# Performance work log

Hardware: AMD Instinct MI355X
Metric: run time of the kernel (lower is better)

## Reference

```python
import jax, jax.numpy as jnp
import numpy as np

N, K, E = 50000, 8, 800000
HID, OUT, DIM_PE, DIM_IN, DIM_EMB = 64, 16, 16, 64, 128

def setup_inputs() -> dict:
    key = jax.random.key(0)
    ks = jax.random.split(key, 16)
    s = 0.05
    inp = {
        "eigvecs": jax.random.normal(ks[0], (N, K), jnp.float32),
        "x": jax.random.normal(ks[1], (N, DIM_IN), jnp.float32),
        "edge_index": jax.random.randint(ks[2], (2, E), 0, N, jnp.int32),
        "batch_index": jnp.sort(jax.random.randint(ks[3], (N,), 0, 8, jnp.int32)),
        # GIN layer 0: MLP(1 -> HID, 1 layer) == single Linear
        "W0": jax.random.normal(ks[4], (1, HID), jnp.float32) * s,
        "b0": jnp.zeros((HID,), jnp.float32),
        # GIN layer 1: MLP(HID -> HID, 1 layer)
        "W1": jax.random.normal(ks[5], (HID, HID), jnp.float32) * s,
        "b1": jnp.zeros((HID,), jnp.float32),
        # GIN layer 2: MLP(HID -> HID -> OUT, 2 layers, relu between)
        "W2a": jax.random.normal(ks[6], (HID, HID), jnp.float32) * s,
        "b2a": jnp.zeros((HID,), jnp.float32),
        "W2b": jax.random.normal(ks[7], (HID, OUT), jnp.float32) * s,
        "b2b": jnp.zeros((OUT,), jnp.float32),
        # rho: MLP(OUT*K -> HID -> DIM_PE, 2 layers)
        "Wr1": jax.random.normal(ks[8], (OUT * K, HID), jnp.float32) * s,
        "br1": jnp.zeros((HID,), jnp.float32),
        "Wr2": jax.random.normal(ks[9], (HID, DIM_PE), jnp.float32) * s,
        "br2": jnp.zeros((DIM_PE,), jnp.float32),
        # linear_x: dim_in -> dim_emb - dim_pe
        "Wx": jax.random.normal(ks[10], (DIM_IN, DIM_EMB - DIM_PE), jnp.float32) * s,
        "bx": jnp.zeros((DIM_EMB - DIM_PE,), jnp.float32),
    }
    return inp

def reference(eigvecs, x, edge_index, batch_index,
              W0, b0, W1, b1, W2a, b2a, W2b, b2b,
              Wr1, br1, Wr2, br2, Wx, bx):
    src, dst = edge_index[0], edge_index[1]

    def agg(h):
        # GINConv sum aggregation: out[i] = h[i] + sum_{(j->i) in E} h[j]  (eps=0)
        return h + jax.ops.segment_sum(h[src], dst, num_segments=N)

    def enc(p):
        # p: [N, K, C]; Linear acts on last dim, message passing on node dim 0
        h = agg(p) @ W0 + b0                       # GINConv(MLP 1-layer): [N,K,HID]
        h = agg(h) @ W1 + b1                       # GINConv(MLP 1-layer)
        m = agg(h)
        return jax.nn.relu(m @ W2a + b2a) @ W2b + b2b  # GINConv(MLP 2-layer): [N,K,OUT]

    # pos_enc = eigvecs.unsqueeze(-1), NaN -> 0
    pos = jnp.nan_to_num(eigvecs)[:, :, None]      # [N,K,1]
    pe = enc(pos) + enc(-pos)                      # sign-invariant sum: [N,K,OUT]
    pe = pe.reshape(N, K * OUT)                    # [N, K*OUT]
    pe = jax.nn.relu(pe @ Wr1 + br1) @ Wr2 + br2   # rho MLP: [N, DIM_PE]

    h = x.astype(jnp.float32) @ Wx + bx            # expand_x linear: [N, DIM_EMB-DIM_PE]
    return jnp.concatenate([h, pe], axis=1)        # [N, DIM_EMB]
```

## Files before the change

### kernel.cpp

```cpp
#include <hip/hip_runtime.h>

__global__ void smallvec_k(const float* __restrict__ W0, const float* __restrict__ b0,
                           const float* __restrict__ W1, const float* __restrict__ b1,
                           const float* __restrict__ W2a, float* __restrict__ SV) {
  __shared__ float w01[64], g[64];
  int j = threadIdx.x;
  float a = 0.f, bg = 0.f;
  for (int i = 0; i < 64; ++i) { float w = W1[i*64 + j]; a += W0[i]*w; bg += b0[i]*w; }
  w01[j] = a; g[j] = bg;
  __syncthreads();
  float w012 = 0.f, P = 0.f, Q = 0.f;
  for (int i = 0; i < 64; ++i) { float w = W2a[i*64 + j]; w012 += w01[i]*w; P += g[i]*w; Q += b1[i]*w; }
  SV[j] = w012; SV[64 + j] = P; SV[128 + j] = Q;
}

__global__ void zero_k(int* __restrict__ p, int n) {
  int i = blockIdx.x * blockDim.x + threadIdx.x;
  if (i < n) p[i] = 0;
}

__global__ void hist_k(const int* __restrict__ ei, int* __restrict__ cnt, int E) {
  int e = blockIdx.x * blockDim.x + threadIdx.x;
  if (e < E) atomicAdd(&cnt[ei[E + e]], 1);
}

__global__ void scan_k(int* __restrict__ ptr, int* __restrict__ cur, int N) {
  __shared__ int sums[256];
  int t = threadIdx.x;
  int chunk = (N + 255) / 256;
  int lo = t * chunk, hi = lo + chunk; if (hi > N) hi = N; if (lo > N) lo = N;
  int s = 0;
  for (int i = lo; i < hi; ++i) s += ptr[i];
  sums[t] = s;
  __syncthreads();
  for (int off = 1; off < 256; off <<= 1) {
    int v = (t >= off) ? sums[t - off] : 0;
    __syncthreads();
    sums[t] += v;
    __syncthreads();
  }
  int run = sums[t] - s;
  for (int i = lo; i < hi; ++i) {
    int c = ptr[i];
    ptr[i] = run; cur[i] = run;
    run += c;
  }
  if (t == 255) ptr[N] = run;
}

__global__ void fill_k(const int* __restrict__ ei, int* __restrict__ cur,
                       int* __restrict__ csr, int E) {
  int e = blockIdx.x * blockDim.x + threadIdx.x;
  if (e >= E) return;
  int s = ei[e], d = ei[E + e];
  int pos = atomicAdd(&cur[d], 1);
  csr[pos] = s;
}

#define RED16(v) { v += __shfl_down(v, 8, 16); v += __shfl_down(v, 4, 16); \
                   v += __shfl_down(v, 2, 16); v += __shfl_down(v, 1, 16); }
#define NANFIX4(u) { u.x = (u.x!=u.x)?0.f:u.x; u.y = (u.y!=u.y)?0.f:u.y; \
                     u.z = (u.z!=u.z)?0.f:u.z; u.w = (u.w!=u.w)?0.f:u.w; }

template<int MODE>
__global__ __launch_bounds__(256) void aggv_k(
    const int* __restrict__ ptr, const int* __restrict__ csr,
    const float* __restrict__ Fin, const float* __restrict__ Din,
    float* __restrict__ Fout, float* __restrict__ Dout, int N) {
  int g = blockIdx.x * 16 + (threadIdx.x >> 4);
  int t = threadIdx.x & 15;
  if (g >= N) return;
  int lo = ptr[g], hi = ptr[g + 1];
  float a0=0.f,a1=0.f,a2=0.f,a3=0.f,a4=0.f,a5=0.f,a6=0.f,a7=0.f,dd=0.f;
  for (int j = lo + t; j < hi; j += 16) {
    int s = csr[j];
    const float* r = Fin + (size_t)s * 8;
    float4 u0 = *(const float4*)r;
    float4 u1 = *(const float4*)(r + 4);
    if (MODE == 0) { NANFIX4(u0); NANFIX4(u1); }
    a0 += u0.x; a1 += u0.y; a2 += u0.z; a3 += u0.w;
    a4 += u1.x; a5 += u1.y; a6 += u1.z; a7 += u1.w;
    if (MODE == 1) dd += Din[s];
  }
  RED16(a0); RED16(a1); RED16(a2); RED16(a3);
  RED16(a4); RED16(a5); RED16(a6); RED16(a7);
  if (MODE == 1) RED16(dd);
  if (t == 0) {
    const float* r = Fin + (size_t)g * 8;
    float4 s0 = *(const float4*)r;
    float4 s1 = *(const float4*)(r + 4);
    if (MODE == 0) { NANFIX4(s0); NANFIX4(s1); }
    float4 o0 = { a0 + s0.x, a1 + s0.y, a2 + s0.z, a3 + s0.w };
    float4 o1 = { a4 + s1.x, a5 + s1.y, a6 + s1.z, a7 + s1.w };
    *(float4*)(Fout + (size_t)g * 8)     = o0;
    *(float4*)(Fout + (size_t)g * 8 + 4) = o1;
    if (MODE == 0) Dout[g] = 1.f + (float)(hi - lo);
    if (MODE == 1) Dout[g] = Din[g] + dd;
  }
}

__global__ __launch_bounds__(256) void pe_k(
    const float* __restrict__ B3, const float* __restrict__ D1, const float* __restrict__ D2,
    const float* __restrict__ SV, const float* __restrict__ b2a,
    const float* __restrict__ W2b, const float* __restrict__ b2b,
    const float* __restrict__ Wr1, const float* __restrict__ br1,
    const float* __restrict__ Wr2, const float* __restrict__ br2,
    float* __restrict__ out, int N) {
  __shared__ float vbuf[4][8][68];
  __shared__ float pebuf[4][128];
  __shared__ float zbuf[4][64];
  int wid  = threadIdx.x >> 6;
  int lane = threadIdx.x & 63;
  int n = blockIdx.x * 4 + wid;
  bool active = (n < N);
  float d1 = 0.f, d2 = 0.f;
  if (active) { d1 = D1[n]; d2 = D2[n]; }
  float w012 = SV[lane], P = SV[64 + lane], Q = SV[128 + lane];
  float Ej = d2 * P + d1 * Q + b2a[lane];
  if (active) {
    #pragma unroll
    for (int k = 0; k < 8; ++k) {
      float s = B3[(size_t)n*8 + k];
      float t = s * w012;
      vbuf[wid][k][lane] = fmaxf(t + Ej, 0.f) + fmaxf(Ej - t, 0.f);
    }
  }
  __syncthreads();
  if (active) {
    #pragma unroll
    for (int cc = 0; cc < 2; ++cc) {
      int c = lane + cc * 64;
      int k = c >> 4, o = c & 15;
      float acc = 2.f * b2b[o];
      #pragma unroll 8
      for (int j = 0; j < 64; ++j) acc += vbuf[wid][k][j] * W2b[j*16 + o];
      pebuf[wid][c] = acc;
    }
  }
  __syncthreads();
  float acc = br1[lane];
  if (active) {
    #pragma unroll 8
    for (int c = 0; c < 128; ++c) acc += pebuf[wid][c] * Wr1[c*64 + lane];
    zbuf[wid][lane] = fmaxf(acc, 0.f);
  }
  __syncthreads();
  if (active && lane < 16) {
    float acc2 = br2[lane];
    #pragma unroll 8
    for (int h = 0; h < 64; ++h) acc2 += zbuf[wid][h] * Wr2[h*16 + lane];
    out[(size_t)n*128 + 112 + lane] = acc2;
  }
}

__global__ void x_k(const float* __restrict__ x, const float* __restrict__ Wx,
                    const float* __restrict__ bx, float* __restrict__ out, int total) {
  int idx = blockIdx.x * blockDim.x + threadIdx.x;
  if (idx >= total) return;
  int n = idx / 112, o = idx % 112;
  const float* xr = x + (size_t)n * 64;
  float acc = bx[o];
  #pragma unroll 8
  for (int i = 0; i < 64; ++i) acc += xr[i] * Wx[i*112 + o];
  out[(size_t)n*128 + o] = acc;
}

extern "C" void kernel_launch(void* const* d_in, const int* in_sizes, int n_in,
                              void* d_out, int out_size, void* d_ws, size_t ws_size,
                              hipStream_t stream) {
  const float* eig = (const float*)d_in[0];
  const float* x   = (const float*)d_in[1];
  const int*   ei  = (const int*)d_in[2];
  const float* W0  = (const float*)d_in[4];
  const float* b0  = (const float*)d_in[5];
  const float* W1  = (const float*)d_in[6];
  const float* b1  = (const float*)d_in[7];
  const float* W2a = (const float*)d_in[8];
  const float* b2a = (const float*)d_in[9];
  const float* W2b = (const float*)d_in[10];
  const float* b2b = (const float*)d_in[11];
  const float* Wr1 = (const float*)d_in[12];
  const float* br1 = (const float*)d_in[13];
  const float* Wr2 = (const float*)d_in[14];
  const float* br2 = (const float*)d_in[15];
  const float* Wx  = (const float*)d_in[16];
  const float* bx  = (const float*)d_in[17];
  float* out = (float*)d_out;

  int N = in_sizes[0] / 8;
  int E = in_sizes[2] / 2;

  int* ptr = (int*)d_ws;
  int* cur = ptr + (N + 1);
  int* csr = cur + N;
  uintptr_t p = (uintptr_t)(csr + E);
  p = (p + 255) & ~(uintptr_t)255;
  float* B1 = (float*)p;
  float* B2 = B1 + (size_t)N * 8;
  float* B3 = B2 + (size_t)N * 8;
  float* D1 = B3 + (size_t)N * 8;
  float* D2 = D1 + N;
  float* SV = D2 + N;

  int eblocks = (E + 255) / 256;
  int nblocks16 = (N + 15) / 16;

  zero_k<<<(N + 256) / 256, 256, 0, stream>>>(ptr, N + 1);
  hist_k<<<eblocks, 256, 0, stream>>>(ei, ptr, E);
  scan_k<<<1, 256, 0, stream>>>(ptr, cur, N);
  fill_k<<<eblocks, 256, 0, stream>>>(ei, cur, csr, E);

  smallvec_k<<<1, 64, 0, stream>>>(W0, b0, W1, b1, W2a, SV);

  aggv_k<0><<<nblocks16, 256, 0, stream>>>(ptr, csr, eig, nullptr, B1, D1, N);
  aggv_k<1><<<nblocks16, 256, 0, stream>>>(ptr, csr, B1, D1, B2, D2, N);
  aggv_k<2><<<nblocks16, 256, 0, stream>>>(ptr, csr, B2, nullptr, B3, nullptr, N);

  pe_k<<<(N + 3) / 4, 256, 0, stream>>>(B3, D1, D2, SV, b2a, W2b, b2b,
                                        Wr1, br1, Wr2, br2, out, N);
  x_k<<<(N * 112 + 255) / 256, 256, 0, stream>>>(x, Wx, bx, out, N * 112);
}
```

Measured before the change: 544.2 us.

## Fuse x-linear into PE kernel, tile 16 nodes per block, fold smallvec into scan

Merges the tiny weight-precompute kernel into the single-block scan kernel and folds the expand_x linear into the PE kernel, removing two launches. The PE kernel now handles 16 nodes per block, 4 per wavefront. It stages transposed W2b and Wr2 in shared memory and reuses each Wr1 and Wx weight load across 4 nodes. It also drops the intra-wave __syncthreads and simplifies relu(E+t)+relu(E-t) to max(2E, E+|t|, 0). More registers and shared memory per block may lower occupancy.

```diff
diff --git a/kernel.cpp b/kernel.cpp
--- a/kernel.cpp
+++ b/kernel.cpp
@@ -1,18 +1,4 @@
 #include <hip/hip_runtime.h>
-
-__global__ void smallvec_k(const float* __restrict__ W0, const float* __restrict__ b0,
-                           const float* __restrict__ W1, const float* __restrict__ b1,
-                           const float* __restrict__ W2a, float* __restrict__ SV) {
-  __shared__ float w01[64], g[64];
-  int j = threadIdx.x;
-  float a = 0.f, bg = 0.f;
-  for (int i = 0; i < 64; ++i) { float w = W1[i*64 + j]; a += W0[i]*w; bg += b0[i]*w; }
-  w01[j] = a; g[j] = bg;
-  __syncthreads();
-  float w012 = 0.f, P = 0.f, Q = 0.f;
-  for (int i = 0; i < 64; ++i) { float w = W2a[i*64 + j]; w012 += w01[i]*w; P += g[i]*w; Q += b1[i]*w; }
-  SV[j] = w012; SV[64 + j] = P; SV[128 + j] = Q;
-}
 
 __global__ void zero_k(int* __restrict__ p, int n) {
   int i = blockIdx.x * blockDim.x + threadIdx.x;
@@ -24,14 +10,23 @@
   if (e < E) atomicAdd(&cnt[ei[E + e]], 1);
 }
 
-__global__ void scan_k(int* __restrict__ ptr, int* __restrict__ cur, int N) {
+__global__ void scan_k(int* __restrict__ ptr, int* __restrict__ cur, int N,
+                       const float* __restrict__ W0, const float* __restrict__ b0,
+                       const float* __restrict__ W1, const float* __restrict__ b1,
+                       const float* __restrict__ W2a, float* __restrict__ SV) {
   __shared__ int sums[256];
+  __shared__ float w01[64], g[64];
   int t = threadIdx.x;
   int chunk = (N + 255) / 256;
   int lo = t * chunk, hi = lo + chunk; if (hi > N) hi = N; if (lo > N) lo = N;
   int s = 0;
   for (int i = lo; i < hi; ++i) s += ptr[i];
   sums[t] = s;
+  if (t < 64) {
+    float a = 0.f, bg = 0.f;
+    for (int i = 0; i < 64; ++i) { float w = W1[i*64 + t]; a += W0[i]*w; bg += b0[i]*w; }
+    w01[t] = a; g[t] = bg;
+  }
   __syncthreads();
   for (int off = 1; off < 256; off <<= 1) {
     int v = (t >= off) ? sums[t - off] : 0;
@@ -46,6 +41,11 @@
     run += c;
   }
   if (t == 255) ptr[N] = run;
+  if (t < 64) {
+    float w012 = 0.f, P = 0.f, Q = 0.f;
+    for (int i = 0; i < 64; ++i) { float w = W2a[i*64 + t]; w012 += w01[i]*w; P += g[i]*w; Q += b1[i]*w; }
+    SV[t] = w012; SV[64 + t] = P; SV[128 + t] = Q;
+  }
 }
 
 __global__ void fill_k(const int* __restrict__ ei, int* __restrict__ cur,
@@ -105,64 +105,118 @@
     const float* __restrict__ W2b, const float* __restrict__ b2b,
     const float* __restrict__ Wr1, const float* __restrict__ br1,
     const float* __restrict__ Wr2, const float* __restrict__ br2,
+    const float* __restrict__ x, const float* __restrict__ Wx,
+    const float* __restrict__ bx,
     float* __restrict__ out, int N) {
+  __shared__ float w2bT[16][68];
+  __shared__ float wr2T[16][68];
   __shared__ float vbuf[4][8][68];
-  __shared__ float pebuf[4][128];
-  __shared__ float zbuf[4][64];
-  int wid  = threadIdx.x >> 6;
-  int lane = threadIdx.x & 63;
-  int n = blockIdx.x * 4 + wid;
-  bool active = (n < N);
-  float d1 = 0.f, d2 = 0.f;
-  if (active) { d1 = D1[n]; d2 = D2[n]; }
-  float w012 = SV[lane], P = SV[64 + lane], Q = SV[128 + lane];
-  float Ej = d2 * P + d1 * Q + b2a[lane];
-  if (active) {
+  __shared__ float pebuf[16][128];
+  __shared__ float zbuf[16][68];
+  int tid = threadIdx.x;
+  int wid = tid >> 6, lane = tid & 63;
+
+  for (int u = tid; u < 1024; u += 256) {
+    int j = u >> 4, o = u & 15;
+    w2bT[o][j] = W2b[u];
+    wr2T[o][j] = Wr2[u];
+  }
+  __syncthreads();
+
+  int nb = blockIdx.x * 16 + wid * 4;
+  float w012 = SV[lane], P = SV[64 + lane], Q = SV[128 + lane], b2aj = b2a[lane];
+  int o16 = lane & 15, kk = lane >> 4;
+  float bb2 = 2.f * b2b[o16];
+  float br1h = br1[lane];
+
+  #pragma unroll
+  for (int m = 0; m < 4; ++m) {
+    int n = nb + m;
+    int nc = (n < N) ? n : 0;
+    float d1 = D1[nc], d2 = D2[nc];
+    float E = fmaf(d2, P, fmaf(d1, Q, b2aj));
+    float E2 = E + E;
+    const float* srow = B3 + (size_t)nc * 8;
     #pragma unroll
     for (int k = 0; k < 8; ++k) {
-      float s = B3[(size_t)n*8 + k];
-      float t = s * w012;
-      vbuf[wid][k][lane] = fmaxf(t + Ej, 0.f) + fmaxf(Ej - t, 0.f);
-    }
-  }
-  __syncthreads();
-  if (active) {
-    #pragma unroll
-    for (int cc = 0; cc < 2; ++cc) {
-      int c = lane + cc * 64;
-      int k = c >> 4, o = c & 15;
-      float acc = 2.f * b2b[o];
-      #pragma unroll 8
-      for (int j = 0; j < 64; ++j) acc += vbuf[wid][k][j] * W2b[j*16 + o];
-      pebuf[wid][c] = acc;
-    }
-  }
-  __syncthreads();
-  float acc = br1[lane];
-  if (active) {
-    #pragma unroll 8
-    for (int c = 0; c < 128; ++c) acc += pebuf[wid][c] * Wr1[c*64 + lane];
-    zbuf[wid][lane] = fmaxf(acc, 0.f);
-  }
-  __syncthreads();
-  if (active && lane < 16) {
-    float acc2 = br2[lane];
-    #pragma unroll 8
-    for (int h = 0; h < 64; ++h) acc2 += zbuf[wid][h] * Wr2[h*16 + lane];
-    out[(size_t)n*128 + 112 + lane] = acc2;
-  }
-}
-
-__global__ void x_k(const float* __restrict__ x, const float* __restrict__ Wx,
-                    const float* __restrict__ bx, float* __restrict__ out, int total) {
-  int idx = blockIdx.x * blockDim.x + threadIdx.x;
-  if (idx >= total) return;
-  int n = idx / 112, o = idx % 112;
-  const float* xr = x + (size_t)n * 64;
-  float acc = bx[o];
+      float t = srow[k] * w012;
+      vbuf[wid][k][lane] = fmaxf(fmaxf(E2, E + fabsf(t)), 0.f);
+    }
+    float accA = bb2, accB = bb2;
+    #pragma unroll
+    for (int j4 = 0; j4 < 16; ++j4) {
+      float4 w4 = *(const float4*)&w2bT[o16][4 * j4];
+      float4 va = *(const float4*)&vbuf[wid][kk][4 * j4];
+      float4 vb = *(const float4*)&vbuf[wid][kk + 4][4 * j4];
+      accA += va.x * w4.x + va.y * w4.y + va.z * w4.z + va.w * w4.w;
+      accB += vb.x * w4.x + vb.y * w4.y + vb.z * w4.z + vb.w * w4.w;
+    }
+    pebuf[wid * 4 + m][lane]      = accA;
+    pebuf[wid * 4 + m][lane + 64] = accB;
+  }
+
+  float za[4] = { br1h, br1h, br1h, br1h };
   #pragma unroll 8
-  for (int i = 0; i < 64; ++i) acc += xr[i] * Wx[i*112 + o];
-  out[(size_t)n*128 + o] = acc;
+  for (int c4 = 0; c4 < 32; ++c4) {
+    float w0 = Wr1[(4 * c4 + 0) * 64 + lane];
+    float w1 = Wr1[(4 * c4 + 1) * 64 + lane];
+    float w2 = Wr1[(4 * c4 + 2) * 64 + lane];
+    float w3 = Wr1[(4 * c4 + 3) * 64 + lane];
+    #pragma unroll
+    for (int m = 0; m < 4; ++m) {
+      float4 p = *(const float4*)&pebuf[wid * 4 + m][4 * c4];
+      za[m] += p.x * w0 + p.y * w1 + p.z * w2 + p.w * w3;
+    }
+  }
+  #pragma unroll
+  for (int m = 0; m < 4; ++m) zbuf[wid * 4 + m][lane] = fmaxf(za[m], 0.f);
+
+  float acc2 = br2[o16];
+  #pragma unroll
+  for (int h4 = 0; h4 < 16; ++h4) {
+    float4 zv = *(const float4*)&zbuf[wid * 4 + kk][4 * h4];
+    float4 wv = *(const float4*)&wr2T[o16][4 * h4];
+    acc2 += zv.x * wv.x + zv.y * wv.y + zv.z * wv.z + zv.w * wv.w;
+  }
+  {
+    int nn = nb + kk;
+    if (nn < N) out[(size_t)nn * 128 + 112 + o16] = acc2;
+  }
+
+  float bxa = bx[lane];
+  float bxb = (lane < 48) ? bx[lane + 64] : 0.f;
+  float xacc[4][2];
+  #pragma unroll
+  for (int m = 0; m < 4; ++m) { xacc[m][0] = bxa; xacc[m][1] = bxb; }
+  #pragma unroll 4
+  for (int i4 = 0; i4 < 16; ++i4) {
+    float4 xv[4];
+    #pragma unroll
+    for (int m = 0; m < 4; ++m) {
+      int nc = (nb + m < N) ? (nb + m) : 0;
+      xv[m] = *(const float4*)(x + (size_t)nc * 64 + 4 * i4);
+    }
+    #pragma unroll
+    for (int i = 0; i < 4; ++i) {
+      int row = 4 * i4 + i;
+      float wa = Wx[row * 112 + lane];
+      float wb = (lane < 48) ? Wx[row * 112 + lane + 64] : 0.f;
+      #pragma unroll
+      for (int m = 0; m < 4; ++m) {
+        float xs = ((const float*)&xv[m])[i];
+        xacc[m][0] = fmaf(xs, wa, xacc[m][0]);
+        xacc[m][1] = fmaf(xs, wb, xacc[m][1]);
+      }
+    }
+  }
+  #pragma unroll
+  for (int m = 0; m < 4; ++m) {
+    int n = nb + m;
+    if (n < N) {
+      out[(size_t)n * 128 + lane] = xacc[m][0];
+      if (lane < 48) out[(size_t)n * 128 + lane + 64] = xacc[m][1];
+    }
+  }
 }
 
 extern "C" void kernel_launch(void* const* d_in, const int* in_sizes, int n_in,
@@ -207,16 +261,13 @@
 
   zero_k<<<(N + 256) / 256, 256, 0, stream>>>(ptr, N + 1);
   hist_k<<<eblocks, 256, 0, stream>>>(ei, ptr, E);
-  scan_k<<<1, 256, 0, stream>>>(ptr, cur, N);
+  scan_k<<<1, 256, 0, stream>>>(ptr, cur, N, W0, b0, W1, b1, W2a, SV);
   fill_k<<<eblocks, 256, 0, stream>>>(ei, cur, csr, E);
-
-  smallvec_k<<<1, 64, 0, stream>>>(W0, b0, W1, b1, W2a, SV);
 
   aggv_k<0><<<nblocks16, 256, 0, stream>>>(ptr, csr, eig, nullptr, B1, D1, N);
   aggv_k<1><<<nblocks16, 256, 0, stream>>>(ptr, csr, B1, D1, B2, D2, N);
   aggv_k<2><<<nblocks16, 256, 0, stream>>>(ptr, csr, B2, nullptr, B3, nullptr, N);
 
-  pe_k<<<(N + 3) / 4, 256, 0, stream>>>(B3, D1, D2, SV, b2a, W2b, b2b,
-                                        Wr1, br1, Wr2, br2, out, N);
-  x_k<<<(N * 112 + 255) / 256, 256, 0, stream>>>(x, Wx, bx, out, N * 112);
-}
+  pe_k<<<nblocks16, 256, 0, stream>>>(B3, D1, D2, SV, b2a, W2b, b2b,
+                                      Wr1, br1, Wr2, br2, x, Wx, bx, out, N);
+}
```

After: 472.0 us. 1.15x faster.
